# Kernel tuning notes

Measured on AMD Instinct MI355X. Metric: run time of the kernel, lower is better.

## Reference

```python
import jax, jax.numpy as jnp
import numpy as np

N = 4096   # out_features (rows of W)
M = 4096   # in_features (cols of W)
S_L = 2048 # Givens pairs on rows
S_R = 2048 # Givens pairs on cols
T = 8192   # tokens (batch*seq)
EPS = 1e-6


def _disjoint_pairs(key, n_feat, n_pairs):
    perm = jax.random.permutation(key, n_feat)[: 2 * n_pairs]
    return perm.reshape(n_pairs, 2).astype(jnp.int32)


def setup_inputs() -> dict:
    key = jax.random.key(0)
    ks = jax.random.split(key, 8)
    x = jax.random.normal(ks[0], (T, M), dtype=jnp.float32)
    W = 0.02 * jax.random.normal(ks[1], (N, M), dtype=jnp.float32)
    bias = jnp.zeros((N,), dtype=jnp.float32)
    theta_L = 0.002 * jax.random.normal(ks[2], (S_L,), dtype=jnp.float32)
    theta_R = 0.002 * jax.random.normal(ks[3], (S_R,), dtype=jnp.float32)
    pairs_L = _disjoint_pairs(ks[4], N, S_L)
    pairs_R = _disjoint_pairs(ks[5], M, S_R)
    ecd_log_mag = jnp.zeros((N,), dtype=jnp.float32)
    base_row_norms = jnp.linalg.norm(W, axis=1)  # [N], captured at init
    return {"x": x, "W": W, "bias": bias, "theta_L": theta_L,
            "theta_R": theta_R, "ecd_log_mag": ecd_log_mag,
            "base_row_norms": base_row_norms, "pairs_L": pairs_L,
            "pairs_R": pairs_R}


def _rotate_rows(Wm, pairs, theta):
    # Disjoint Givens rotations on rows: gather pair rows, 2x2 rotate, scatter.
    i, j = pairs[:, 0], pairs[:, 1]
    c = jnp.cos(theta)[:, None]
    s = jnp.sin(theta)[:, None]
    ri, rj = Wm[i], Wm[j]              # [S, M] gathers
    return Wm.at[i].set(c * ri - s * rj).at[j].set(s * ri + c * rj)


def _rotate_cols(Wm, pairs, theta):
    i, j = pairs[:, 0], pairs[:, 1]
    c = jnp.cos(theta)[None, :]
    s = jnp.sin(theta)[None, :]
    ci, cj = Wm[:, i], Wm[:, j]        # [N, S] gathers
    return Wm.at[:, i].set(c * ci - s * cj).at[:, j].set(s * ci + c * cj)


def reference(x, W, bias, theta_L, theta_R, ecd_log_mag, base_row_norms,
              pairs_L, pairs_R):
    # Effective weight: W_eff = G_L(theta_L) @ W @ G_R(theta_R)^T
    W_eff = _rotate_rows(_rotate_cols(W, pairs_R, theta_R), pairs_L, theta_L)
    # Magnitude (ECD) rescaling: restore base per-row norms modulated by
    # learned log-magnitudes.
    row_norms = jnp.sqrt(jnp.sum(W_eff * W_eff, axis=1) + EPS)  # [N]
    scale = base_row_norms * jnp.exp(ecd_log_mag) / row_norms   # [N]
    W_eff = W_eff * scale[:, None]
    return x @ W_eff.T + bias
```

## Files before the change

### kernel.cpp

```cpp
#include <hip/hip_runtime.h>
#include <cstdint>
#include <cstddef>

constexpr int T_N = 8192;
constexpr int MM  = 4096;
constexpr int NN  = 4096;
constexpr int S_L = 2048;
constexpr int S_R = 2048;
constexpr float EPS_ = 1e-6f;

typedef float  f32x4   __attribute__((ext_vector_type(4)));
typedef __bf16 bf16x8  __attribute__((ext_vector_type(8)));
typedef unsigned short ushort8 __attribute__((ext_vector_type(8)));

__device__ __forceinline__ unsigned short f2bf(float f) {
  unsigned int u = __float_as_uint(f);
  u += 0x7FFFu + ((u >> 16) & 1u);
  return (unsigned short)(u >> 16);
}

__global__ void init_cols(float* colC, float* colS, int* colP) {
  int i = blockIdx.x * blockDim.x + threadIdx.x;
  if (i < MM) { colC[i] = 1.f; colS[i] = 0.f; colP[i] = i; }
}

__global__ void build_cols(const float* __restrict__ thR, const int* __restrict__ prR,
                           float* colC, float* colS, int* colP) {
  int s = blockIdx.x * blockDim.x + threadIdx.x;
  if (s < S_R) {
    int i = prR[2*s], j = prR[2*s+1];
    float c = cosf(thR[s]), sn = sinf(thR[s]);
    colC[i] = c; colS[i] = -sn; colP[i] = j;
    colC[j] = c; colS[j] =  sn; colP[j] = i;
  }
}

__global__ __launch_bounds__(256) void weff_conv(
    const float* __restrict__ W, const float* __restrict__ brn, const float* __restrict__ elm,
    const float* __restrict__ thL, const int* __restrict__ prL,
    const float* __restrict__ colC, const float* __restrict__ colS, const int* __restrict__ colP,
    unsigned short* __restrict__ Wb,
    const float* __restrict__ x, unsigned short* __restrict__ xb)
{
  __shared__ __align__(16) float rI[MM];
  __shared__ __align__(16) float rJ[MM];
  __shared__ float red[8];

  int bid = blockIdx.x;
  int tid = threadIdx.x;

  if (bid >= S_L) {
    const size_t total = (size_t)T_N * MM / 8;
    for (size_t i = (size_t)(bid - S_L) * 256 + tid; i < total; i += 2048ull * 256ull) {
      const float* s = x + i * 8;
      f32x4 v0 = *(const f32x4*)s;
      f32x4 v1 = *(const f32x4*)(s + 4);
      ushort8 p;
      p[0] = f2bf(v0.x); p[1] = f2bf(v0.y); p[2] = f2bf(v0.z); p[3] = f2bf(v0.w);
      p[4] = f2bf(v1.x); p[5] = f2bf(v1.y); p[6] = f2bf(v1.z); p[7] = f2bf(v1.w);
      *(ushort8*)(xb + i * 8) = p;
    }
    return;
  }

  int s = bid;
  int i = prL[2*s], j = prL[2*s+1];
  float cl = cosf(thL[s]), sl = sinf(thL[s]);
  const float* Wi = W + (size_t)i * MM;
  const float* Wj = W + (size_t)j * MM;

  for (int m = tid * 4; m < MM; m += 1024) {
    *(f32x4*)&rI[m] = *(const f32x4*)&Wi[m];
    *(f32x4*)&rJ[m] = *(const f32x4*)&Wj[m];
  }
  __syncthreads();

  float ssi = 0.f, ssj = 0.f;
  for (int m = tid; m < MM; m += 256) {
    int p = colP[m];
    float c = colC[m], sn = colS[m];
    float vi = c * rI[m] + sn * rI[p];
    float vj = c * rJ[m] + sn * rJ[p];
    float ei = cl * vi - sl * vj;
    float ej = sl * vi + cl * vj;
    ssi += ei * ei;
    ssj += ej * ej;
  }
  #pragma unroll
  for (int o = 32; o; o >>= 1) { ssi += __shfl_xor(ssi, o); ssj += __shfl_xor(ssj, o); }
  int lane = tid & 63, wid = tid >> 6;
  if (lane == 0) { red[wid] = ssi; red[4 + wid] = ssj; }
  __syncthreads();
  float ti = red[0] + red[1] + red[2] + red[3];
  float tj = red[4] + red[5] + red[6] + red[7];
  float sci = brn[i] * expf(elm[i]) / sqrtf(ti + EPS_);
  float scj = brn[j] * expf(elm[j]) / sqrtf(tj + EPS_);

  for (int m0 = tid * 8; m0 < MM; m0 += 2048) {
    ushort8 pi, pj;
    #pragma unroll
    for (int q = 0; q < 8; q++) {
      int m = m0 + q;
      int p = colP[m];
      float c = colC[m], sn = colS[m];
      float vi = c * rI[m] + sn * rI[p];
      float vj = c * rJ[m] + sn * rJ[p];
      pi[q] = f2bf((cl * vi - sl * vj) * sci);
      pj[q] = f2bf((sl * vi + cl * vj) * scj);
    }
    *(ushort8*)&Wb[(size_t)i * MM + m0] = pi;
    *(ushort8*)&Wb[(size_t)j * MM + m0] = pj;
  }
}

typedef const __attribute__((address_space(1))) unsigned int* as1_u32p;
typedef __attribute__((address_space(3))) unsigned int* as3_u32p;

__device__ __forceinline__ void gl_lds16(const void* g, void* l) {
  __builtin_amdgcn_global_load_lds((as1_u32p)g, (as3_u32p)l, 16, 0, 0);
}

constexpr int GBM = 256, GBN = 256, GBK = 64;
constexpr int NTK = MM / GBK;
constexpr int BUFB = GBM * GBK * 2;

#define SB0() __builtin_amdgcn_sched_barrier(0)
#define BAR() __builtin_amdgcn_s_barrier()
#define LGKM0() do { asm volatile("s_waitcnt lgkmcnt(0)" ::: "memory"); \
                     SB0(); } while (0)

#define RD_A8(DST, AB, MIH)                                                   \
  _Pragma("unroll") for (int i_ = 0; i_ < 4; ++i_)                            \
  _Pragma("unroll") for (int k_ = 0; k_ < 2; ++k_)                            \
    DST[i_][k_] = *(const bf16x8*)((AB) + arow0 + ((MIH) * 4 + i_) * 2048     \
                                    + ((k_ * 64 + lg * 16) ^ sw));

#define RD_B4(DST, BB, NIH)                                                   \
  _Pragma("unroll") for (int n_ = 0; n_ < 2; ++n_)                            \
  _Pragma("unroll") for (int k_ = 0; k_ < 2; ++k_)                            \
    DST[n_][k_] = *(const bf16x8*)((BB) + brow0 + ((NIH) * 2 + n_) * 2048     \
                                    + ((k_ * 64 + lg * 16) ^ sw));

#define QMF(AF, BF, MI0, NI0)                                                 \
  __builtin_amdgcn_s_setprio(1);                                              \
  _Pragma("unroll") for (int k_ = 0; k_ < 2; ++k_)                            \
  _Pragma("unroll") for (int i_ = 0; i_ < 4; ++i_)                            \
  _Pragma("unroll") for (int n_ = 0; n_ < 2; ++n_)                            \
    acc[(MI0) + i_][(NI0) + n_] = __builtin_amdgcn_mfma_f32_16x16x32_bf16(    \
        AF[i_][k_], BF[n_][k_], acc[(MI0) + i_][(NI0) + n_], 0, 0, 0);        \
  __builtin_amdgcn_s_setprio(0);

#define STG_A(KOF, BUF, H)                                                    \
  _Pragma("unroll") for (int l_ = 2 * (H); l_ < 2 * (H) + 2; ++l_)            \
    gl_lds16(sA + (size_t)l_ * (64 * MM) + (KOF),                             \
             ldsA + (BUF) * BUFB + dstb + l_ * 8192);
#define STG_B(KOF, BUF, H)                                                    \
  _Pragma("unroll") for (int l_ = 2 * (H); l_ < 2 * (H) + 2; ++l_)            \
    gl_lds16(sB + (size_t)l_ * (64 * MM) + (KOF),                             \
             ldsB + (BUF) * BUFB + dstb + l_ * 8192);

#define GATE4x asm volatile("s_waitcnt vmcnt(4)" ::: "memory")
#define GATE0x asm volatile("s_waitcnt vmcnt(0)" ::: "memory")
#define GNONE  do { } while (0)

#define TILEX(T, BB, a0C, b0C, a0N, b0N, DOB1, DOT2, GATE3, DORDN)            \
  {                                                                           \
    const char* Ab_  = ldsA + (BB) * BUFB;                                    \
    const char* Bb_  = ldsB + (BB) * BUFB;                                    \
    const char* AbN_ = ldsA + ((BB) ^ 1) * BUFB;                              \
    const char* BbN_ = ldsB + ((BB) ^ 1) * BUFB;                              \
    bf16x8 a1[4][2], b1[2][2];                                                \
                         \
    LGKM0();                                                                  \
    RD_A8(a1, Ab_, 1);                                                        \
    SB0();                                                                    \
    QMF(a0C, b0C, 0, 0);                                                      \
    if (DOB1) { STG_B(((T) + 1) * GBK, (BB) ^ 1, 1); }                        \
    BAR();                                                                    \
                            \
    LGKM0();                                                                  \
    RD_B4(b1, Bb_, 1);                                                        \
    SB0();                                                                    \
    QMF(a1, b0C, 4, 0);                                                       \
    if (DOT2) { STG_B(((T) + 2) * GBK, (BB), 0); }                            \
    BAR();                                                                    \
                            \
    LGKM0();                                                                  \
    QMF(a1, b1, 4, 2);                                                        \
    if (DOT2) { STG_A(((T) + 2) * GBK, (BB), 0); }                            \
    GATE3;                                                                    \
    BAR();                                                                    \
                 \
    if (DORDN) { RD_B4(b0N, BbN_, 0); RD_A8(a0N, AbN_, 0); SB0(); }           \
    QMF(a0C, b1, 0, 2);                                                       \
    if (DOT2) { STG_A(((T) + 2) * GBK, (BB), 1); }                            \
    BAR();                                                                    \
  }

__global__ __launch_bounds__(512, 2) void gemm8(
    const unsigned short* __restrict__ xb,
    const unsigned short* __restrict__ wb,
    const float* __restrict__ bias,
    float* __restrict__ C)
{
  __shared__ __align__(16) unsigned short As[2 * GBM * GBK];
  __shared__ __align__(16) unsigned short Bs[2 * GBN * GBK];
  char* ldsA = (char*)As;
  char* ldsB = (char*)Bs;

  int bid = blockIdx.x;
  int swz = (bid & 7) * 64 + (bid >> 3);
  int tn = swz & 15, tm = swz >> 4;
  const int trow0 = tm * GBM;
  const int tcol0 = tn * GBN;

  int tid  = threadIdx.x;
  int lane = tid & 63;
  int wid  = tid >> 6;
  int wr = wid >> 2, wc = wid & 3;
  int lr = lane & 15;
  int lg = lane >> 4;
  const int sw = (lr & 7) << 4;
  const int arow0 = (wr * 128 + lr) * 128;
  const int brow0 = (wc * 64  + lr) * 128;

  const int r0   = tid >> 3;
  const int colg = (tid & 7) ^ (r0 & 7);
  const unsigned short* sA = xb + (size_t)(trow0 + r0) * MM + colg * 8;
  const unsigned short* sB = wb + (size_t)(tcol0 + r0) * MM + colg * 8;
  const int dstb = tid * 16;

  f32x4 acc[8][4];
  #pragma unroll
  for (int i = 0; i < 8; i++)
    #pragma unroll
    for (int j = 0; j < 4; j++) {
      f32x4 z = {0.f, 0.f, 0.f, 0.f};
      acc[i][j] = z;
    }

  STG_A(0, 0, 0); STG_A(0, 0, 1); STG_B(0, 0, 0); STG_B(0, 0, 1);
  STG_B(GBK, 1, 0); STG_A(GBK, 1, 0); STG_A(GBK, 1, 1);
  asm volatile("s_waitcnt vmcnt(6)" ::: "memory");
  __builtin_amdgcn_s_barrier();

  bf16x8 a0A[4][2], b0A[2][2], a0B[4][2], b0B[2][2];
  RD_B4(b0A, ldsB, 0);
  RD_A8(a0A, ldsA, 0);

  #pragma unroll 1
  for (int t = 0; t < NTK - 2; t += 2) {
    TILEX(t,     0, a0A, b0A, a0B, b0B, 1, 1, GATE4x, 1);
    TILEX(t + 1, 1, a0B, b0B, a0A, b0A, 1, 1, GATE4x, 1);
  }
  TILEX(NTK - 2, 0, a0A, b0A, a0B, b0B, 1, 0, GATE0x, 1);
  TILEX(NTK - 1, 1, a0B, b0B, a0A, b0A, 0, 0, GNONE, 0);

  #pragma unroll
  for (int ni = 0; ni < 4; ++ni) {
    int col = tcol0 + wc * 64 + ni * 16 + lr;
    float bi = bias[col];
    #pragma unroll
    for (int mi = 0; mi < 8; ++mi) {
      int rr0 = trow0 + wr * 128 + mi * 16 + lg * 4;
      #pragma unroll
      for (int qq = 0; qq < 4; ++qq)
        C[(size_t)(rr0 + qq) * NN + col] = acc[mi][ni][qq] + bi;
    }
  }
}

constexpr int BM = 128, BN = 128, BK = 64;

__global__ __launch_bounds__(256) void gemm_fb(
    const float* __restrict__ xf,
    const unsigned short* __restrict__ wb, const float* __restrict__ bias,
    float* __restrict__ C)
{
  __shared__ __align__(16) unsigned short As2[BM * BK];
  __shared__ __align__(16) unsigned short Bs2[BN * BK];

  int bid = blockIdx.x;
  int swz = (bid & 7) * 256 + (bid >> 3);
  int tn = swz & 31;
  int tm = swz >> 5;

  int tid  = threadIdx.x;
  int lane = tid & 63;
  int wid  = tid >> 6;
  int wr = wid >> 1, wc = wid & 1;
  int lr = lane & 15;
  int lg = lane >> 4;

  f32x4 acc[4][4];
  #pragma unroll
  for (int i = 0; i < 4; i++)
    #pragma unroll
    for (int j = 0; j < 4; j++) {
      f32x4 z = {0.f, 0.f, 0.f, 0.f};
      acc[i][j] = z;
    }

  int srow = tid >> 3;
  int scol = (tid & 7) * 8;
  const size_t a_base = (size_t)(tm * BM) * MM;
  const size_t b_base = (size_t)(tn * BN) * MM;

  for (int k0 = 0; k0 < MM; k0 += BK) {
    #pragma unroll
    for (int c = 0; c < 4; c++) {
      int row = c * 32 + srow;
      gl_lds16(wb + b_base + (size_t)row * MM + k0 + scol,
               (char*)Bs2 + (c * 256 + wid * 64) * 16);
    }
    #pragma unroll
    for (int c = 0; c < 4; c++) {
      int row = c * 32 + srow;
      const float* s = xf + a_base + (size_t)row * MM + k0 + scol;
      f32x4 v0 = *(const f32x4*)s;
      f32x4 v1 = *(const f32x4*)(s + 4);
      ushort8 p;
      p[0] = f2bf(v0.x); p[1] = f2bf(v0.y); p[2] = f2bf(v0.z); p[3] = f2bf(v0.w);
      p[4] = f2bf(v1.x); p[5] = f2bf(v1.y); p[6] = f2bf(v1.z); p[7] = f2bf(v1.w);
      *(ushort8*)&As2[(c * 256 + tid) * 8] = p;
    }
    __syncthreads();

    #pragma unroll
    for (int kk = 0; kk < 2; kk++) {
      bf16x8 a[4], b[4];
      #pragma unroll
      for (int i = 0; i < 4; i++) {
        a[i] = *(const bf16x8*)&As2[(wr * 64 + i * 16 + lr) * BK + kk * 32 + lg * 8];
        b[i] = *(const bf16x8*)&Bs2[(wc * 64 + i * 16 + lr) * BK + kk * 32 + lg * 8];
      }
      #pragma unroll
      for (int i = 0; i < 4; i++)
        #pragma unroll
        for (int j = 0; j < 4; j++)
          acc[i][j] = __builtin_amdgcn_mfma_f32_16x16x32_bf16(a[i], b[j], acc[i][j], 0, 0, 0);
    }
    __syncthreads();
  }

  int gn0 = tn * BN + wc * 64;
  int gt0 = tm * BM + wr * 64;
  #pragma unroll
  for (int j = 0; j < 4; j++) {
    int gn = gn0 + j * 16 + lr;
    float bi = bias[gn];
    #pragma unroll
    for (int i = 0; i < 4; i++) {
      int t0 = gt0 + i * 16 + lg * 4;
      #pragma unroll
      for (int q = 0; q < 4; q++)
        C[(size_t)(t0 + q) * NN + gn] = acc[i][j][q] + bi;
    }
  }
}

extern "C" void kernel_launch(void* const* d_in, const int* in_sizes, int n_in,
                              void* d_out, int out_size, void* d_ws, size_t ws_size,
                              hipStream_t stream)
{
  const float* x    = (const float*)d_in[0];
  const float* W    = (const float*)d_in[1];
  const float* bias = (const float*)d_in[2];
  const float* thL  = (const float*)d_in[3];
  const float* thR  = (const float*)d_in[4];
  const float* elm  = (const float*)d_in[5];
  const float* brn  = (const float*)d_in[6];
  const int*   prL  = (const int*)d_in[7];
  const int*   prR  = (const int*)d_in[8];
  float* out = (float*)d_out;

  char* ws = (char*)d_ws;
  unsigned short* Wb = (unsigned short*)ws;
  size_t off = (size_t)NN * MM * 2;
  float* colC = (float*)(ws + off); off += MM * 4;
  float* colS = (float*)(ws + off); off += MM * 4;
  int*   colP = (int*)  (ws + off); off += MM * 4;
  unsigned short* xb = (unsigned short*)(ws + off);
  bool use_xb = ws_size >= off + (size_t)T_N * MM * 2;

  init_cols <<<16, 256, 0, stream>>>(colC, colS, colP);
  build_cols<<< 8, 256, 0, stream>>>(thR, prR, colC, colS, colP);

  if (use_xb) {
    weff_conv<<<S_L + 2048, 256, 0, stream>>>(W, brn, elm, thL, prL,
                                              colC, colS, colP, Wb, x, xb);
    gemm8<<<512, 512, 0, stream>>>(xb, Wb, bias, out);
  } else {
    weff_conv<<<S_L, 256, 0, stream>>>(W, brn, elm, thL, prL,
                                       colC, colS, colP, Wb, x, xb);
    gemm_fb<<<2048, 256, 0, stream>>>(x, Wb, bias, out);
  }
}
```

Measured before the change: 312.1 us.

## Replace 8-wave GEMM with 4-wave 128x128-per-wave kernel and simpler double buffering

The bf16 GEMM moves from 512 threads (8 waves, each computing a 128x64 subtile) to 256 threads (4 waves, each computing a 128x128 subtile with 64 accumulators). The K loop becomes a plain double-buffered loop with fine-grained lgkmcnt waits that interleave LDS reads with MFMAs, and global-to-LDS staging is spread through the iteration. The aim is more MFMA work per LDS fragment read and lower barrier overhead. In exchange, register pressure is much higher (about 256 accumulator VGPRs), occupancy drops to one block per CU, and a full vmcnt(0) wait plus barrier at the end of each iteration may expose memory latency.

```diff
diff --git a/kernel.cpp b/kernel.cpp
--- a/kernel.cpp
+++ b/kernel.cpp
@@ -126,78 +126,32 @@
 
 #define SB0() __builtin_amdgcn_sched_barrier(0)
 #define BAR() __builtin_amdgcn_s_barrier()
-#define LGKM0() do { asm volatile("s_waitcnt lgkmcnt(0)" ::: "memory"); \
-                     SB0(); } while (0)
-
-#define RD_A8(DST, AB, MIH)                                                   \
-  _Pragma("unroll") for (int i_ = 0; i_ < 4; ++i_)                            \
-  _Pragma("unroll") for (int k_ = 0; k_ < 2; ++k_)                            \
-    DST[i_][k_] = *(const bf16x8*)((AB) + arow0 + ((MIH) * 4 + i_) * 2048     \
-                                    + ((k_ * 64 + lg * 16) ^ sw));
-
-#define RD_B4(DST, BB, NIH)                                                   \
-  _Pragma("unroll") for (int n_ = 0; n_ < 2; ++n_)                            \
-  _Pragma("unroll") for (int k_ = 0; k_ < 2; ++k_)                            \
-    DST[n_][k_] = *(const bf16x8*)((BB) + brow0 + ((NIH) * 2 + n_) * 2048     \
-                                    + ((k_ * 64 + lg * 16) ^ sw));
-
-#define QMF(AF, BF, MI0, NI0)                                                 \
-  __builtin_amdgcn_s_setprio(1);                                              \
-  _Pragma("unroll") for (int k_ = 0; k_ < 2; ++k_)                            \
-  _Pragma("unroll") for (int i_ = 0; i_ < 4; ++i_)                            \
-  _Pragma("unroll") for (int n_ = 0; n_ < 2; ++n_)                            \
-    acc[(MI0) + i_][(NI0) + n_] = __builtin_amdgcn_mfma_f32_16x16x32_bf16(    \
-        AF[i_][k_], BF[n_][k_], acc[(MI0) + i_][(NI0) + n_], 0, 0, 0);        \
-  __builtin_amdgcn_s_setprio(0);
-
-#define STG_A(KOF, BUF, H)                                                    \
-  _Pragma("unroll") for (int l_ = 2 * (H); l_ < 2 * (H) + 2; ++l_)            \
-    gl_lds16(sA + (size_t)l_ * (64 * MM) + (KOF),                             \
-             ldsA + (BUF) * BUFB + dstb + l_ * 8192);
-#define STG_B(KOF, BUF, H)                                                    \
-  _Pragma("unroll") for (int l_ = 2 * (H); l_ < 2 * (H) + 2; ++l_)            \
-    gl_lds16(sB + (size_t)l_ * (64 * MM) + (KOF),                             \
-             ldsB + (BUF) * BUFB + dstb + l_ * 8192);
-
-#define GATE4x asm volatile("s_waitcnt vmcnt(4)" ::: "memory")
-#define GATE0x asm volatile("s_waitcnt vmcnt(0)" ::: "memory")
-#define GNONE  do { } while (0)
-
-#define TILEX(T, BB, a0C, b0C, a0N, b0N, DOB1, DOT2, GATE3, DORDN)            \
-  {                                                                           \
-    const char* Ab_  = ldsA + (BB) * BUFB;                                    \
-    const char* Bb_  = ldsB + (BB) * BUFB;                                    \
-    const char* AbN_ = ldsA + ((BB) ^ 1) * BUFB;                              \
-    const char* BbN_ = ldsB + ((BB) ^ 1) * BUFB;                              \
-    bf16x8 a1[4][2], b1[2][2];                                                \
-                         \
-    LGKM0();                                                                  \
-    RD_A8(a1, Ab_, 1);                                                        \
-    SB0();                                                                    \
-    QMF(a0C, b0C, 0, 0);                                                      \
-    if (DOB1) { STG_B(((T) + 1) * GBK, (BB) ^ 1, 1); }                        \
-    BAR();                                                                    \
-                            \
-    LGKM0();                                                                  \
-    RD_B4(b1, Bb_, 1);                                                        \
-    SB0();                                                                    \
-    QMF(a1, b0C, 4, 0);                                                       \
-    if (DOT2) { STG_B(((T) + 2) * GBK, (BB), 0); }                            \
-    BAR();                                                                    \
-                            \
-    LGKM0();                                                                  \
-    QMF(a1, b1, 4, 2);                                                        \
-    if (DOT2) { STG_A(((T) + 2) * GBK, (BB), 0); }                            \
-    GATE3;                                                                    \
-    BAR();                                                                    \
-                 \
-    if (DORDN) { RD_B4(b0N, BbN_, 0); RD_A8(a0N, AbN_, 0); SB0(); }           \
-    QMF(a0C, b1, 0, 2);                                                       \
-    if (DOT2) { STG_A(((T) + 2) * GBK, (BB), 1); }                            \
-    BAR();                                                                    \
-  }
-
-__global__ __launch_bounds__(512, 2) void gemm8(
+#define LGKMN(N) do { asm volatile("s_waitcnt lgkmcnt(" #N ")" ::: "memory"); \
+                      SB0(); } while (0)
+#define VMC0() asm volatile("s_waitcnt vmcnt(0)" ::: "memory")
+
+#define MFK(M, N, K)                                                          \
+  acc[M][N] = __builtin_amdgcn_mfma_f32_16x16x32_bf16(a[M][K], b[N][K],       \
+                                                      acc[M][N], 0, 0, 0);
+
+#define NISTEP(N)                                                             \
+  MFK(0, N, 0) MFK(1, N, 0) MFK(2, N, 0) MFK(3, N, 0)                         \
+  MFK(4, N, 0) MFK(5, N, 0) MFK(6, N, 0) MFK(7, N, 0)                         \
+  MFK(0, N, 1) MFK(1, N, 1) MFK(2, N, 1) MFK(3, N, 1)                         \
+  MFK(4, N, 1) MFK(5, N, 1) MFK(6, N, 1) MFK(7, N, 1)
+
+#define RDB(N)                                                                \
+  b[N][0] = *(const bf16x8*)(bK0 + (N) * 2048);                               \
+  b[N][1] = *(const bf16x8*)(bK1 + (N) * 2048);                               \
+  SB0();
+
+#define STGC(KOF, AN, BN, CC)                                                 \
+  gl_lds16(sA + (size_t)(2*(CC))   * (32 * MM) + (KOF), (AN) + dstb + (2*(CC))   * 4096); \
+  gl_lds16(sA + (size_t)(2*(CC)+1) * (32 * MM) + (KOF), (AN) + dstb + (2*(CC)+1) * 4096); \
+  gl_lds16(sB + (size_t)(2*(CC))   * (32 * MM) + (KOF), (BN) + dstb + (2*(CC))   * 4096); \
+  gl_lds16(sB + (size_t)(2*(CC)+1) * (32 * MM) + (KOF), (BN) + dstb + (2*(CC)+1) * 4096);
+
+__global__ __launch_bounds__(256, 1) void gemm4(
     const unsigned short* __restrict__ xb,
     const unsigned short* __restrict__ wb,
     const float* __restrict__ bias,
@@ -216,13 +170,15 @@
 
   int tid  = threadIdx.x;
   int lane = tid & 63;
-  int wid  = tid >> 6;
-  int wr = wid >> 2, wc = wid & 3;
+  int wv   = tid >> 6;
+  int wr = wv >> 1, wc = wv & 1;
   int lr = lane & 15;
   int lg = lane >> 4;
   const int sw = (lr & 7) << 4;
+  const int koff0 = (lg * 16) ^ sw;
+  const int koff1 = (64 + lg * 16) ^ sw;
   const int arow0 = (wr * 128 + lr) * 128;
-  const int brow0 = (wc * 64  + lr) * 128;
+  const int brow0 = (wc * 128 + lr) * 128;
 
   const int r0   = tid >> 3;
   const int colg = (tid & 7) ^ (r0 & 7);
@@ -230,35 +186,91 @@
   const unsigned short* sB = wb + (size_t)(tcol0 + r0) * MM + colg * 8;
   const int dstb = tid * 16;
 
-  f32x4 acc[8][4];
+  f32x4 acc[8][8];
   #pragma unroll
   for (int i = 0; i < 8; i++)
     #pragma unroll
-    for (int j = 0; j < 4; j++) {
+    for (int j = 0; j < 8; j++) {
       f32x4 z = {0.f, 0.f, 0.f, 0.f};
       acc[i][j] = z;
     }
 
-  STG_A(0, 0, 0); STG_A(0, 0, 1); STG_B(0, 0, 0); STG_B(0, 0, 1);
-  STG_B(GBK, 1, 0); STG_A(GBK, 1, 0); STG_A(GBK, 1, 1);
-  asm volatile("s_waitcnt vmcnt(6)" ::: "memory");
-  __builtin_amdgcn_s_barrier();
-
-  bf16x8 a0A[4][2], b0A[2][2], a0B[4][2], b0B[2][2];
-  RD_B4(b0A, ldsB, 0);
-  RD_A8(a0A, ldsA, 0);
+  {
+    char* A0 = ldsA; char* B0 = ldsB;
+    STGC(0, A0, B0, 0) STGC(0, A0, B0, 1) STGC(0, A0, B0, 2) STGC(0, A0, B0, 3)
+  }
+  VMC0();
+  BAR();
 
   #pragma unroll 1
-  for (int t = 0; t < NTK - 2; t += 2) {
-    TILEX(t,     0, a0A, b0A, a0B, b0B, 1, 1, GATE4x, 1);
-    TILEX(t + 1, 1, a0B, b0B, a0A, b0A, 1, 1, GATE4x, 1);
-  }
-  TILEX(NTK - 2, 0, a0A, b0A, a0B, b0B, 1, 0, GATE0x, 1);
-  TILEX(NTK - 1, 1, a0B, b0B, a0A, b0A, 0, 0, GNONE, 0);
+  for (int t = 0; t < NTK; ++t) {
+    const int cur = t & 1;
+    char* Anxt = ldsA + (cur ^ 1) * BUFB;
+    char* Bnxt = ldsB + (cur ^ 1) * BUFB;
+    const char* aK0 = ldsA + cur * BUFB + arow0 + koff0;
+    const char* aK1 = ldsA + cur * BUFB + arow0 + koff1;
+    const char* bK0 = ldsB + cur * BUFB + brow0 + koff0;
+    const char* bK1 = ldsB + cur * BUFB + brow0 + koff1;
+    const int kof1 = (t + 1) * GBK;
+    const bool st = (t + 1 < NTK);
+
+    bf16x8 a[8][2], b[8][2];
+
+    RDB(0)
+    #pragma unroll
+    for (int m = 0; m < 8; ++m) {
+      a[m][0] = *(const bf16x8*)(aK0 + m * 2048);
+      a[m][1] = *(const bf16x8*)(aK1 + m * 2048);
+      SB0();
+    }
+    RDB(1)
+    if (st) { STGC(kof1, Anxt, Bnxt, 0) }
+    SB0();
+
+    LGKMN(15); MFK(0, 0, 0)
+    LGKMN(14); MFK(1, 0, 0)
+    LGKMN(12); MFK(2, 0, 0)
+    LGKMN(10); MFK(3, 0, 0)
+    LGKMN(8);  MFK(4, 0, 0)
+    LGKMN(6);  MFK(5, 0, 0)
+    LGKMN(4);  MFK(6, 0, 0)
+    LGKMN(2);  MFK(7, 0, 0)
+    MFK(0, 0, 1) MFK(1, 0, 1) MFK(2, 0, 1) MFK(3, 0, 1)
+    MFK(4, 0, 1) MFK(5, 0, 1) MFK(6, 0, 1) MFK(7, 0, 1)
+    RDB(2)
+    if (st) { STGC(kof1, Anxt, Bnxt, 1) }
+    SB0();
+
+    LGKMN(2);  NISTEP(1)
+    RDB(3)
+    if (st) { STGC(kof1, Anxt, Bnxt, 2) }
+    SB0();
+
+    LGKMN(2);  NISTEP(2)
+    RDB(4)
+    if (st) { STGC(kof1, Anxt, Bnxt, 3) }
+    SB0();
+
+    LGKMN(2);  NISTEP(3)
+    RDB(5)
+
+    LGKMN(2);  NISTEP(4)
+    RDB(6)
+
+    LGKMN(2);  NISTEP(5)
+    RDB(7)
+
+    LGKMN(2);  NISTEP(6)
+
+    LGKMN(0);  NISTEP(7)
+
+    if (st) { VMC0(); }
+    BAR();
+  }
 
   #pragma unroll
-  for (int ni = 0; ni < 4; ++ni) {
-    int col = tcol0 + wc * 64 + ni * 16 + lr;
+  for (int ni = 0; ni < 8; ++ni) {
+    int col = tcol0 + wc * 128 + ni * 16 + lr;
     float bi = bias[col];
     #pragma unroll
     for (int mi = 0; mi < 8; ++mi) {
@@ -389,7 +401,7 @@
   if (use_xb) {
     weff_conv<<<S_L + 2048, 256, 0, stream>>>(W, brn, elm, thL, prL,
                                               colC, colS, colP, Wb, x, xb);
-    gemm8<<<512, 512, 0, stream>>>(xb, Wb, bias, out);
+    gemm4<<<512, 256, 0, stream>>>(xb, Wb, bias, out);
   } else {
     weff_conv<<<S_L, 256, 0, stream>>>(W, brn, elm, thL, prL,
                                        colC, colS, colP, Wb, x, xb);
```

Result: slower. 423.1 us (+35.6%).
